# Kernel optimization log

Hardware: AMD Instinct MI355X
Metric: run time of the kernel (lower is better)

## Reference

```python
import jax, jax.numpy as jnp
import numpy as np

# DeepSeek-V3-style gate config
TOP_K = 8
N_EXPERTS = 256
N_GROUP = 8
TOPK_GROUP = 4
ROUTED_SCALING = 2.5
EPS = 1e-20


def setup_inputs() -> dict:
    key = jax.random.key(0)
    k1, k2, k3 = jax.random.split(key, 3)
    S, H = 16384, 7168
    hidden_states = jax.random.normal(k1, (S, H), dtype=jnp.float32)
    weight = jax.random.normal(k2, (N_EXPERTS, H), dtype=jnp.float32) * 0.02
    e_score_correction_bias = jax.random.normal(k3, (N_EXPERTS,), dtype=jnp.float32) * 0.1
    return {"hidden_states": hidden_states, "weight": weight,
            "e_score_correction_bias": e_score_correction_bias}


def reference(hidden_states, weight, e_score_correction_bias):
    S = hidden_states.shape[0]
    group_size = N_EXPERTS // N_GROUP  # 32

    # gating GEMM: [S, E]
    router_logits = jnp.einsum('sh,eh->se', hidden_states, weight)
    # scoring_func == 'sigmoid'
    scores = jax.nn.sigmoid(router_logits)
    scores_for_choice = scores + e_score_correction_bias[None, :]

    # group scores: sum of top-2 biased scores within each group -> [S, G]
    grouped = scores_for_choice.reshape(S, N_GROUP, group_size)
    top2_vals, _ = jax.lax.top_k(grouped, 2)
    group_scores = top2_vals.sum(axis=-1)

    # select top `TOPK_GROUP` groups, build group mask
    _, group_idx = jax.lax.top_k(group_scores, TOPK_GROUP)  # [S, topk_group]
    group_mask = jnp.zeros((S, N_GROUP), dtype=scores.dtype)
    group_mask = group_mask.at[jnp.arange(S)[:, None], group_idx].set(1.0)
    score_mask = jnp.repeat(group_mask, group_size, axis=-1)  # [S, E]

    # masked top-k over experts; weights gathered from UNBIASED scores
    tmp_scores = jnp.where(score_mask > 0, scores_for_choice, 0.0)
    _, topk_idx = jax.lax.top_k(tmp_scores, TOP_K)  # [S, top_k]
    topk_weight = jnp.take_along_axis(scores, topk_idx, axis=1)

    # renormalize (top_k > 1 and norm_topk_prob) then scale (noaux_tc)
    denom = topk_weight.sum(axis=-1, keepdims=True) + EPS
    topk_weight = topk_weight / denom * ROUTED_SCALING
    return topk_weight, topk_idx
```

## Files before the change

kernel.cpp:

```cpp
#include <hip/hip_runtime.h>
#include <math.h>

#define H_DIM 7168
#define N_EXP 256
#define N_GRP 8
#define G_SZ  32
#define TOPK_G 4
#define TOPK   8
#define BM 64
#define BK 32
#define S_TOK 16384
#define NTILES (H_DIM / BK)
#define NTH    (NTILES / 2)
#define TILE_W_BYTES 32768

#define SA_SCALE 256.0f
#define SW_SCALE 4096.0f
#define DESCALE  (1.0f / 1048576.0f)

__device__ __align__(256) char g_wimg[(size_t)NTILES * TILE_W_BYTES];
__device__ __align__(256) float g_part[2 * (size_t)S_TOK * N_EXP];

typedef __attribute__((ext_vector_type(8))) _Float16 f16x8;
typedef __attribute__((ext_vector_type(4))) float f32x4;
typedef __attribute__((ext_vector_type(4))) unsigned short u16x4;
typedef __attribute__((ext_vector_type(8))) unsigned short u16x8;

__device__ inline void split2h(float x, unsigned short& h, unsigned short& l) {
    _Float16 hf = (_Float16)x;
    _Float16 lf = (_Float16)(x - (float)hf);
    h = __builtin_bit_cast(unsigned short, hf);
    l = __builtin_bit_cast(unsigned short, lf);
}

__global__ __launch_bounds__(256)
void convert_w_kernel(const float* __restrict__ W) {
    int idx  = blockIdx.x * 256 + threadIdx.x;
    int e    = idx / (H_DIM / 8);
    int koct = idx - e * (H_DIM / 8);
    int k0   = koct * 8;
    int t    = k0 >> 5;
    int o    = (k0 >> 3) & 3;
    int lane = (e & 15) | (o << 4);
    int w    = e >> 5;
    int nj   = (e >> 4) & 1;
    const float* src = W + (size_t)e * H_DIM + k0;
    unsigned short h[8], l[8];
    #pragma unroll
    for (int j = 0; j < 8; ++j)
        split2h(src[j] * SW_SCALE, h[j], l[j]);
    char* base = g_wimg + (size_t)t * TILE_W_BYTES + (w << 12) + (lane << 4);
    *(u16x8*)(base + nj * 1024)       = u16x8{h[0],h[1],h[2],h[3],h[4],h[5],h[6],h[7]};
    *(u16x8*)(base + (2 + nj) * 1024) = u16x8{l[0],l[1],l[2],l[3],l[4],l[5],l[6],l[7]};
}

__global__ __launch_bounds__(512, 4)
void moe_gemm_half(const float* __restrict__ A)
{
    __shared__ __align__(128) char smem[16384];

    const int tid   = threadIdx.x;
    const int lane  = tid & 63;
    const int wave  = tid >> 6;
    const int khalf = blockIdx.x & 1;
    const int brow  = (blockIdx.x >> 1) * BM;
    const int g0    = khalf * NTH;

    const int fr   = lane & 15;
    const int fkb  = (lane >> 4) << 4;
    const int fswz = ((fr << 6) + fkb) ^ ((fr & 7) << 4);

    const int ar   = tid >> 3;
    const int akq  = tid & 7;
    const int aswz = ((ar << 6) + (akq << 3)) ^ ((ar & 7) << 4);
    const float4* Ag4 = reinterpret_cast<const float4*>(
        A + (size_t)(brow + ar) * H_DIM + khalf * (H_DIM / 2)) + akq;

    const char* wsrc = g_wimg + (size_t)g0 * TILE_W_BYTES + (wave << 12) + (lane << 4);

    f32x4 acc[4][2] = {};

    auto loadW = [&](int t, f16x8& h0, f16x8& h1, f16x8& l0, f16x8& l1) {
        const char* p = wsrc + (size_t)t * TILE_W_BYTES;
        h0 = *(const f16x8*)(p + 0);
        h1 = *(const f16x8*)(p + 1024);
        l0 = *(const f16x8*)(p + 2048);
        l1 = *(const f16x8*)(p + 3072);
    };

    auto writeA = [&](const float4& v, char* ab) {
        unsigned short h[4], l[4];
        split2h(v.x * SA_SCALE, h[0], l[0]); split2h(v.y * SA_SCALE, h[1], l[1]);
        split2h(v.z * SA_SCALE, h[2], l[2]); split2h(v.w * SA_SCALE, h[3], l[3]);
        *(u16x4*)(ab + aswz)        = u16x4{h[0], h[1], h[2], h[3]};
        *(u16x4*)(ab + 4096 + aswz) = u16x4{l[0], l[1], l[2], l[3]};
    };

    auto compute = [&](const char* ab, f16x8 bh0, f16x8 bh1, f16x8 bl0, f16x8 bl1) {
        f16x8 ah[4], al[4];
        #pragma unroll
        for (int mi = 0; mi < 4; ++mi) {
            ah[mi] = *(const f16x8*)(ab + mi * 1024 + fswz);
            al[mi] = *(const f16x8*)(ab + 4096 + mi * 1024 + fswz);
        }
        #pragma unroll
        for (int mi = 0; mi < 4; ++mi)
            acc[mi][0] = __builtin_amdgcn_mfma_f32_16x16x32_f16(ah[mi], bh0, acc[mi][0], 0, 0, 0);
        #pragma unroll
        for (int mi = 0; mi < 4; ++mi)
            acc[mi][1] = __builtin_amdgcn_mfma_f32_16x16x32_f16(ah[mi], bh1, acc[mi][1], 0, 0, 0);
        #pragma unroll
        for (int mi = 0; mi < 4; ++mi)
            acc[mi][0] = __builtin_amdgcn_mfma_f32_16x16x32_f16(al[mi], bh0, acc[mi][0], 0, 0, 0);
        #pragma unroll
        for (int mi = 0; mi < 4; ++mi)
            acc[mi][1] = __builtin_amdgcn_mfma_f32_16x16x32_f16(al[mi], bh1, acc[mi][1], 0, 0, 0);
        #pragma unroll
        for (int mi = 0; mi < 4; ++mi)
            acc[mi][0] = __builtin_amdgcn_mfma_f32_16x16x32_f16(ah[mi], bl0, acc[mi][0], 0, 0, 0);
        #pragma unroll
        for (int mi = 0; mi < 4; ++mi)
            acc[mi][1] = __builtin_amdgcn_mfma_f32_16x16x32_f16(ah[mi], bl1, acc[mi][1], 0, 0, 0);
    };

    char* ab0 = smem;
    char* ab1 = smem + 8192;

    f16x8 xh0, xh1, xl0, xl1;
    f16x8 yh0, yh1, yl0, yl1;
    loadW(0, xh0, xh1, xl0, xl1);
    loadW(1, yh0, yh1, yl0, yl1);
    float4 aq1 = Ag4[1 * 8], aq2 = Ag4[2 * 8], aq3 = Ag4[3 * 8];
    writeA(Ag4[0], ab0);
    asm volatile("s_waitcnt lgkmcnt(0)" ::: "memory");
    __builtin_amdgcn_s_barrier();

    #pragma unroll 1
    for (int t = 0; t < NTH; t += 2) {
        {
            int tp2 = (t + 2 < NTH) ? t + 2 : NTH - 1;
            int tp4 = (t + 4 < NTH) ? t + 4 : NTH - 1;
            float4 anew = Ag4[(size_t)tp4 * 8];
            f16x8 nh0, nh1, nl0, nl1;
            loadW(tp2, nh0, nh1, nl0, nl1);
            compute(ab0, xh0, xh1, xl0, xl1);
            writeA(aq1, ab1);
            asm volatile("s_waitcnt lgkmcnt(0)" ::: "memory");
            __builtin_amdgcn_s_barrier();
            xh0 = nh0; xh1 = nh1; xl0 = nl0; xl1 = nl1;
            aq1 = aq2; aq2 = aq3; aq3 = anew;
        }
        {
            int tp3 = (t + 3 < NTH) ? t + 3 : NTH - 1;
            int tp5 = (t + 5 < NTH) ? t + 5 : NTH - 1;
            float4 anew = Ag4[(size_t)tp5 * 8];
            f16x8 nh0, nh1, nl0, nl1;
            loadW(tp3, nh0, nh1, nl0, nl1);
            compute(ab1, yh0, yh1, yl0, yl1);
            writeA(aq1, ab0);
            asm volatile("s_waitcnt lgkmcnt(0)" ::: "memory");
            __builtin_amdgcn_s_barrier();
            yh0 = nh0; yh1 = nh1; yl0 = nl0; yl1 = nl1;
            aq1 = aq2; aq2 = aq3; aq3 = anew;
        }
    }

    float* pb = g_part + ((size_t)khalf * S_TOK + brow) * N_EXP;
    #pragma unroll
    for (int mi = 0; mi < 4; ++mi)
        #pragma unroll
        for (int nj = 0; nj < 2; ++nj)
            #pragma unroll
            for (int q = 0; q < 4; ++q) {
                int row = mi * 16 + ((lane >> 4) << 2) + q;
                int col = wave * 32 + nj * 16 + (lane & 15);
                pb[row * N_EXP + col] = acc[mi][nj][q];
            }
}

__global__ __launch_bounds__(256)
void gate_kernel(const float* __restrict__ bias, float* __restrict__ out, int S)
{
    const int lane = threadIdx.x & 63;
    const int row  = (blockIdx.x * 256 + threadIdx.x) >> 6;

    const float4 p0 = *(const float4*)(g_part + (size_t)row * N_EXP + lane * 4);
    const float4 p1 = *(const float4*)(g_part + ((size_t)S_TOK + row) * N_EXP + lane * 4);
    const float4 b4 = *(const float4*)(bias + lane * 4);

    float s[4], v[4];
    float m1 = -1e30f, m2 = -1e30f;
    {
        const float* q0 = (const float*)&p0;
        const float* q1 = (const float*)&p1;
        const float* qb = (const float*)&b4;
        #pragma unroll
        for (int j = 0; j < 4; ++j) {
            float x = (q0[j] + q1[j]) * DESCALE;
            s[j] = 1.0f / (1.0f + expf(-x));
            float sb = s[j] + qb[j];
            v[j] = sb;
            if (sb > m1) { m2 = m1; m1 = sb; } else if (sb > m2) { m2 = sb; }
        }
    }
    #pragma unroll
    for (int d = 1; d < 8; d <<= 1) {
        float om1 = __shfl_xor(m1, d), om2 = __shfl_xor(m2, d);
        float hi = fmaxf(m1, om1), lo = fminf(m1, om1);
        m1 = hi;
        m2 = fmaxf(lo, fmaxf(m2, om2));
    }
    float gs = m1 + m2;
    float gsv[8];
    #pragma unroll
    for (int g = 0; g < 8; ++g) gsv[g] = __shfl(gs, g << 3);

    unsigned gmask = 0;
    #pragma unroll
    for (int t = 0; t < TOPK_G; ++t) {
        float best = -1e30f; int bg = 0;
        #pragma unroll
        for (int g = 0; g < 8; ++g) {
            bool avail = !((gmask >> g) & 1);
            if (avail && gsv[g] > best) { best = gsv[g]; bg = g; }
        }
        gmask |= 1u << bg;
    }

    const bool sel = (gmask >> (lane >> 3)) & 1;
    #pragma unroll
    for (int j = 0; j < 4; ++j) v[j] = sel ? v[j] : 0.0f;

    float wv[TOPK]; int wi[TOPK]; float wsum = 0.0f;
    #pragma unroll
    for (int t = 0; t < TOPK; ++t) {
        float bv = v[0]; int bj = 0;
        #pragma unroll
        for (int j = 1; j < 4; ++j)
            if (v[j] > bv) { bv = v[j]; bj = j; }
        int bidx = (lane << 2) | bj;
        #pragma unroll
        for (int d = 32; d >= 1; d >>= 1) {
            float ov = __shfl_xor(bv, d);
            int   oi = __shfl_xor(bidx, d);
            if (ov > bv || (ov == bv && oi < bidx)) { bv = ov; bidx = oi; }
        }
        int ol = bidx >> 2, oj = bidx & 3;
        float sl = s[0];
        if (oj == 1) sl = s[1]; else if (oj == 2) sl = s[2]; else if (oj == 3) sl = s[3];
        float sv = __shfl(sl, ol);
        wv[t] = sv; wi[t] = bidx; wsum += sv;
        if (lane == ol) {
            if (oj == 0) v[0] = -1e30f; else if (oj == 1) v[1] = -1e30f;
            else if (oj == 2) v[2] = -1e30f; else v[3] = -1e30f;
        }
    }

    if (lane == 0) {
        float scale = 2.5f / (wsum + 1e-20f);
        #pragma unroll
        for (int t = 0; t < TOPK; ++t) {
            out[(size_t)row * TOPK + t] = wv[t] * scale;
            out[(size_t)S * TOPK + (size_t)row * TOPK + t] = (float)wi[t];
        }
    }
}

extern "C" void kernel_launch(void* const* d_in, const int* in_sizes, int n_in,
                              void* d_out, int out_size, void* d_ws, size_t ws_size,
                              hipStream_t stream) {
    const float* A    = (const float*)d_in[0];
    const float* W    = (const float*)d_in[1];
    const float* bias = (const float*)d_in[2];
    float* out = (float*)d_out;
    const int S = in_sizes[0] / H_DIM;

    convert_w_kernel<<<dim3(N_EXP * (H_DIM / 8) / 256), 256, 0, stream>>>(W);
    moe_gemm_half<<<dim3(2 * S / BM), 512, 0, stream>>>(A);
    gate_kernel<<<dim3(S / 4), 256, 0, stream>>>(bias, out, S);
}
```

Baseline: 223.1 us.

## Batch four K-tiles per barrier interval with larger double-buffered LDS

Restructures the GEMM main loop so each synchronisation interval covers four K-tiles instead of one. A tiles for the next interval are loaded into registers up front and written to a second LDS half partway through the current interval, so only one barrier is needed per four tiles. LDS use grows from 16 KB to 64 KB per block, which may cap occupancy below the four blocks per CU in the launch bounds. Holding more A registers in flight also raises register pressure.

```diff
diff --git a/kernel.cpp b/kernel.cpp
--- a/kernel.cpp
+++ b/kernel.cpp
@@ -11,7 +11,10 @@
 #define BK 32
 #define S_TOK 16384
 #define NTILES (H_DIM / BK)
-#define NTH    (NTILES / 2)
+#define NSPLIT 2
+#define NH     (NTILES / NSPLIT)
+#define ITILES 4
+#define NINT   (NH / ITILES)
 #define TILE_W_BYTES 32768
 
 #define SA_SCALE 256.0f
@@ -19,7 +22,7 @@
 #define DESCALE  (1.0f / 1048576.0f)
 
 __device__ __align__(256) char g_wimg[(size_t)NTILES * TILE_W_BYTES];
-__device__ __align__(256) float g_part[2 * (size_t)S_TOK * N_EXP];
+__device__ __align__(256) float g_part[NSPLIT * (size_t)S_TOK * N_EXP];
 
 typedef __attribute__((ext_vector_type(8))) _Float16 f16x8;
 typedef __attribute__((ext_vector_type(4))) float f32x4;
@@ -57,14 +60,14 @@
 __global__ __launch_bounds__(512, 4)
 void moe_gemm_half(const float* __restrict__ A)
 {
-    __shared__ __align__(128) char smem[16384];
+    __shared__ __align__(128) char smem[2 * ITILES * 8192];
 
     const int tid   = threadIdx.x;
     const int lane  = tid & 63;
     const int wave  = tid >> 6;
     const int khalf = blockIdx.x & 1;
     const int brow  = (blockIdx.x >> 1) * BM;
-    const int g0    = khalf * NTH;
+    const int g0    = khalf * NH;
 
     const int fr   = lane & 15;
     const int fkb  = (lane >> 4) << 4;
@@ -74,7 +77,7 @@
     const int akq  = tid & 7;
     const int aswz = ((ar << 6) + (akq << 3)) ^ ((ar & 7) << 4);
     const float4* Ag4 = reinterpret_cast<const float4*>(
-        A + (size_t)(brow + ar) * H_DIM + khalf * (H_DIM / 2)) + akq;
+        A + (size_t)(brow + ar) * H_DIM + khalf * (H_DIM / NSPLIT)) + akq;
 
     const char* wsrc = g_wimg + (size_t)g0 * TILE_W_BYTES + (wave << 12) + (lane << 4);
 
@@ -123,46 +126,50 @@
             acc[mi][1] = __builtin_amdgcn_mfma_f32_16x16x32_f16(ah[mi], bl1, acc[mi][1], 0, 0, 0);
     };
 
-    char* ab0 = smem;
-    char* ab1 = smem + 8192;
-
     f16x8 xh0, xh1, xl0, xl1;
     f16x8 yh0, yh1, yl0, yl1;
-    loadW(0, xh0, xh1, xl0, xl1);
-    loadW(1, yh0, yh1, yl0, yl1);
-    float4 aq1 = Ag4[1 * 8], aq2 = Ag4[2 * 8], aq3 = Ag4[3 * 8];
-    writeA(Ag4[0], ab0);
-    asm volatile("s_waitcnt lgkmcnt(0)" ::: "memory");
-    __builtin_amdgcn_s_barrier();
+
+    {
+        char* b0 = smem;
+        float4 a0[ITILES];
+        #pragma unroll
+        for (int s = 0; s < ITILES; ++s) a0[s] = Ag4[(size_t)s * 8];
+        loadW(0, xh0, xh1, xl0, xl1);
+        loadW(1, yh0, yh1, yl0, yl1);
+        #pragma unroll
+        for (int s = 0; s < ITILES; ++s) writeA(a0[s], b0 + s * 8192);
+        asm volatile("s_waitcnt lgkmcnt(0)" ::: "memory");
+        __builtin_amdgcn_s_barrier();
+    }
 
     #pragma unroll 1
-    for (int t = 0; t < NTH; t += 2) {
-        {
-            int tp2 = (t + 2 < NTH) ? t + 2 : NTH - 1;
-            int tp4 = (t + 4 < NTH) ? t + 4 : NTH - 1;
-            float4 anew = Ag4[(size_t)tp4 * 8];
+    for (int i = 0; i < NINT; ++i) {
+        char* cur = smem + (i & 1) * (ITILES * 8192);
+        char* nxt = smem + ((i + 1) & 1) * (ITILES * 8192);
+        const bool havenext = (i + 1 < NINT);
+        const int ibase = (havenext ? i + 1 : i) * ITILES;
+
+        float4 an[ITILES];
+        #pragma unroll
+        for (int s = 0; s < ITILES; ++s) an[s] = Ag4[(size_t)(ibase + s) * 8];
+
+        #pragma unroll
+        for (int s = 0; s < ITILES; ++s) {
+            const int t = i * ITILES + s;
+            const int tpf = (t + 2 < NH) ? t + 2 : NH - 1;
             f16x8 nh0, nh1, nl0, nl1;
-            loadW(tp2, nh0, nh1, nl0, nl1);
-            compute(ab0, xh0, xh1, xl0, xl1);
-            writeA(aq1, ab1);
-            asm volatile("s_waitcnt lgkmcnt(0)" ::: "memory");
-            __builtin_amdgcn_s_barrier();
-            xh0 = nh0; xh1 = nh1; xl0 = nl0; xl1 = nl1;
-            aq1 = aq2; aq2 = aq3; aq3 = anew;
-        }
-        {
-            int tp3 = (t + 3 < NTH) ? t + 3 : NTH - 1;
-            int tp5 = (t + 5 < NTH) ? t + 5 : NTH - 1;
-            float4 anew = Ag4[(size_t)tp5 * 8];
-            f16x8 nh0, nh1, nl0, nl1;
-            loadW(tp3, nh0, nh1, nl0, nl1);
-            compute(ab1, yh0, yh1, yl0, yl1);
-            writeA(aq1, ab0);
-            asm volatile("s_waitcnt lgkmcnt(0)" ::: "memory");
-            __builtin_amdgcn_s_barrier();
+            loadW(tpf, nh0, nh1, nl0, nl1);
+            compute(cur + s * 8192, xh0, xh1, xl0, xl1);
+            if (s == 1 && havenext) {
+                #pragma unroll
+                for (int ss = 0; ss < ITILES; ++ss)
+                    writeA(an[ss], nxt + ss * 8192);
+            }
+            xh0 = yh0; xh1 = yh1; xl0 = yl0; xl1 = yl1;
             yh0 = nh0; yh1 = nh1; yl0 = nl0; yl1 = nl1;
-            aq1 = aq2; aq2 = aq3; aq3 = anew;
-        }
+        }
+        asm volatile("s_waitcnt lgkmcnt(0)" ::: "memory");
+        __builtin_amdgcn_s_barrier();
     }
 
     float* pb = g_part + ((size_t)khalf * S_TOK + brow) * N_EXP;
@@ -276,6 +283,6 @@
     const int S = in_sizes[0] / H_DIM;
 
     convert_w_kernel<<<dim3(N_EXP * (H_DIM / 8) / 256), 256, 0, stream>>>(W);
-    moe_gemm_half<<<dim3(2 * S / BM), 512, 0, stream>>>(A);
+    moe_gemm_half<<<dim3(NSPLIT * S / BM), 512, 0, stream>>>(A);
     gate_kernel<<<dim3(S / 4), 256, 0, stream>>>(bias, out, S);
 }
```

New measurement: 218.7 us. No clear change (-2.0%).
